# Kernel tuning notes

Hardware: AMD Instinct MI355X
Metric: run time of the kernel (lower is better)

## Reference

```python
import jax, jax.numpy as jnp
import numpy as np

B, N, F, H, E = 32, 512, 256, 1024, 8192
LN_EPS = 1e-5


def setup_inputs() -> dict:
    key = jax.random.key(0)
    ks = jax.random.split(key, 8)
    s = 0.02
    return {
        "node_features": jax.random.normal(ks[0], (B, N, F), jnp.float32),
        "edge_indexd": jax.random.randint(ks[1], (2, E), 0, N, jnp.int64),
        "edge_weights": jax.random.uniform(ks[2], (B, E), jnp.float32),
        "ln_gamma": jnp.ones((F,), jnp.float32),
        "ln_beta": jnp.zeros((F,), jnp.float32),
        "w1": jax.random.normal(ks[3], (H, N), jnp.float32) * s,
        "b1": jnp.zeros((H,), jnp.float32),
        "w2": jax.random.normal(ks[4], (N, H), jnp.float32) * s,
        "b2": jnp.zeros((N,), jnp.float32),
    }


def _laplacian(edge_idx, w):
    # w: [E] edge weights for one graph; edge_idx: [2, E]
    w = jnp.clip(w, 0.0, 1.0)
    # sparse_coo_tensor(...).to_dense() sums duplicate indices -> scatter-add
    A = jnp.zeros((N, N), w.dtype).at[edge_idx[0], edge_idx[1]].add(w)
    A = (A + A.T) * 0.5
    deg = jnp.clip(A.sum(axis=1), 1e-6, None)
    dis = deg ** -0.5  # finite since deg >= 1e-6
    L = jnp.eye(N, dtype=w.dtype) - dis[:, None] * A * dis[None, :]
    L = (L + L.T) * 0.5 + 1e-6 * jnp.eye(N, dtype=w.dtype)
    return L


def _forward(node_features, edge_indexd, edge_weights, ln_gamma, ln_beta, w1, b1, w2, b2):
    L = jax.vmap(lambda w: _laplacian(edge_indexd, w))(edge_weights)  # [B,N,N]
    # eigh is applied to L.detach() in the original -> stop_gradient
    eigvals, eigvecs = jnp.linalg.eigh(jax.lax.stop_gradient(L))  # [B,N], [B,N,N]

    # LayerNorm over feat_dim
    mu = node_features.mean(-1, keepdims=True)
    var = node_features.var(-1, keepdims=True)
    x = (node_features - mu) * jax.lax.rsqrt(var + LN_EPS) * ln_gamma + ln_beta
    x_residual = x
    x = jax.nn.relu(x)

    # x1 = eigvecs^T @ x : [B,N,F]
    x1 = jnp.einsum('bnk,bnf->bkf', eigvecs, x)
    # MLP on eigenvalues (dropout inactive in eval)
    h = jax.nn.relu(eigvals @ w1.T + b1)  # [B,H]
    ev_feat = h @ w2.T + b2               # [B,N]
    x1 = x1 * ev_feat[:, :, None]
    out = jnp.einsum('bnk,bkf->bnf', eigvecs, x1) + x_residual
    return out


def reference(node_features, edge_indexd, edge_weights, ln_gamma, ln_beta, w1, b1, w2, b2):
    return _forward(node_features, edge_indexd, edge_weights, ln_gamma, ln_beta, w1, b1, w2, b2)
```

## Files before the change

kernel.cpp:

```cpp
#include <hip/hip_runtime.h>
#include <math.h>

#define BDIM 32
#define NDIM 512
#define FDIM 256
#define HDIM 1024
#define EDIM 8192
#define PCH  8192
#define CLTH 1.2e-4f
#define NB   16

__device__ __forceinline__ float waveRedSum(float v){
#pragma unroll
  for(int o=32;o>0;o>>=1) v += __shfl_down(v,o,64);
  return v;
}

__device__ __forceinline__ float rnd_f(int g, int i){
  unsigned s = (unsigned)g*1315423911u ^ (unsigned)i*2654435761u;
  s ^= s>>13; s *= 2246822519u; s ^= s>>16;
  return (float)(s & 0xFFFF)*(1.f/65536.f) - 0.5f;
}

__global__ __launch_bounds__(1024) void k_detect(const unsigned* __restrict__ e, int* __restrict__ flag){
  int t = threadIdx.x;
  float c = 0.f;
  for(int i=t;i<EDIM;i+=1024) if(e[2*i+1] != 0u) c += 1.f;
  c = waveRedSum(c);
  __shared__ float r[16];
  if((t&63)==0) r[t>>6]=c;
  __syncthreads();
  if(t==0){ float s=0; for(int z=0;z<16;z++) s+=r[z]; flag[0] = (s>64.f)?1:0; }
}

__global__ __launch_bounds__(256) void k_scatter(const float* __restrict__ ew, const int* __restrict__ eidx,
                                                 const int* __restrict__ flag, float* __restrict__ A){
  int t = blockIdx.x*256 + threadIdx.x;
  int b = t>>13, e = t&(EDIM-1);
  int i, j;
  if(flag[0]){ i = eidx[e]; j = eidx[EDIM+e]; }
  else       { i = eidx[2*e]; j = eidx[2*(EDIM+e)]; }
  i &= 511; j &= 511;
  float w = ew[(size_t)b*EDIM + e];
  w = 0.5f*fminf(fmaxf(w,0.f),1.f);
  float* Ab = A + (size_t)b*NDIM*NDIM;
  atomicAdd(Ab + (size_t)i*NDIM + j, w);
  atomicAdd(Ab + (size_t)j*NDIM + i, w);
}

__global__ __launch_bounds__(256) void k_degree(const float* __restrict__ A, float* __restrict__ dis){
  int wid = threadIdx.x>>6, lane = threadIdx.x&63;
  int row = blockIdx.x*4 + wid;
  const float* Ar = A + (size_t)row*NDIM;
  float s = 0.f;
  for(int j=lane;j<NDIM;j+=64) s += Ar[j];
  s = waveRedSum(s);
  if(lane==0) dis[row] = rsqrtf(fmaxf(s, 1e-6f));
}

__global__ __launch_bounds__(256) void k_lap(float* __restrict__ A, const float* __restrict__ dis){
  size_t t = (size_t)blockIdx.x*256 + threadIdx.x;
  size_t nn = (size_t)NDIM*NDIM;
  int b = (int)(t / nn); size_t rem = t % nn;
  int i = (int)(rem / NDIM), j = (int)(rem % NDIM);
  float v = -dis[b*NDIM+i]*dis[b*NDIM+j]*A[t];
  if(i==j) v += 1.f + 1e-6f;
  A[t] = v;
}

__global__ __launch_bounds__(256) void k_ln(const float* __restrict__ nf, const float* __restrict__ g,
                                            const float* __restrict__ be, float* __restrict__ X){
  int wid = threadIdx.x>>6, lane = threadIdx.x&63;
  int row = blockIdx.x*4 + wid;
  const float4* r4 = (const float4*)(nf + (size_t)row*FDIM);
  float4 v = r4[lane];
  float s  = v.x+v.y+v.z+v.w;
  float s2 = v.x*v.x+v.y*v.y+v.z*v.z+v.w*v.w;
  s = waveRedSum(s); s2 = waveRedSum(s2);
  s = __shfl(s,0,64); s2 = __shfl(s2,0,64);
  float mean = s*(1.f/FDIM);
  float var  = s2*(1.f/FDIM) - mean*mean;
  float inv  = rsqrtf(var + 1e-5f);
  float4 gg = ((const float4*)g)[lane];
  float4 bb = ((const float4*)be)[lane];
  float4 o;
  o.x = (v.x-mean)*inv*gg.x + bb.x;
  o.y = (v.y-mean)*inv*gg.y + bb.y;
  o.z = (v.z-mean)*inv*gg.z + bb.z;
  o.w = (v.w-mean)*inv*gg.w + bb.w;
  ((float4*)(X + (size_t)row*FDIM))[lane] = o;
}

__global__ __launch_bounds__(512,1) void k_tridiag(float* __restrict__ A, float* __restrict__ U,
                                                   float* __restrict__ dia, float* __restrict__ off,
                                                   float* __restrict__ tau){
  const int b = blockIdx.x, t = threadIdx.x;
  float* Ab = A + (size_t)b*NDIM*NDIM;
  float* Ub = U + (size_t)b*NDIM*NDIM;
  __shared__ __align__(16) float Up[NB][NDIM];
  __shared__ __align__(16) float Wp[NB][NDIM];
  __shared__ __align__(16) float ps[4][NDIM];
  __shared__ float dW[NB], dU[NB];
  __shared__ float sig_s, pd_s, x0_s;
  const int lane = t&63;
  const int cc = t&127, rg = t>>7;
  if(t==0){ sig_s = 0.f; pd_s = 0.f; }

  for(int k0=0; k0<NDIM-2; k0+=NB){
    const int ne = (NB < NDIM-2-k0)? NB : (NDIM-2-k0);
    for(int q=0;q<NB;q++){ Up[q][t]=0.f; Wp[q][t]=0.f; }
    __syncthreads();
    for(int p=0;p<ne;p++){
      const int k = k0+p;
      float v = 0.f;
      if(t>k){
        v = Ab[(size_t)k*NDIM + t];
        for(int q=0;q<p;q++) v -= Up[q][k]*Wp[q][t] + Wp[q][k]*Up[q][t];
      }
      if(t<NB){ dW[t]=0.f; dU[t]=0.f; }
      if(t==0) pd_s = 0.f;
      if(t==k+1) x0_s = v;
      float ssq = (t>=k+2)? v*v : 0.f;
      ssq = waveRedSum(ssq);
      if(lane==0) atomicAdd(&sig_s, ssq);
      __syncthreads();
      const float sigma = sig_s, x0 = x0_s;
      float tk = 0.f, inv = 0.f, beta = x0;
      if(sigma > 1e-26f){
        beta = -copysignf(sqrtf(x0*x0+sigma), x0);
        tk = (beta-x0)/beta; inv = 1.f/(x0-beta);
      }
      const float u_t = (t>=k+2)? v*inv : ((t==k+1 && sigma>1e-26f)? 1.f : 0.f);
      Up[p][t] = u_t;
      for(int q=0;q<p;q++){
        float pw = waveRedSum(Wp[q][t]*u_t);
        float pu = waveRedSum(Up[q][t]*u_t);
        if(lane==0){ atomicAdd(&dW[q],pw); atomicAdd(&dU[q],pu); }
      }
      __syncthreads();
      if(t==0) sig_s = 0.f;
      {
        float4 acc = {0.f,0.f,0.f,0.f};
        const int j0 = 4*cc;
        if(j0+3 > k){
          const float* basep = Ab + j0;
          const int ib0 = (k+1)&~15;
          const float* ap = basep + (size_t)(ib0+rg*4)*NDIM;
          float4 c0 = *(const float4*)(ap);
          float4 c1 = *(const float4*)(ap+NDIM);
          float4 c2 = *(const float4*)(ap+2*NDIM);
          float4 c3 = *(const float4*)(ap+3*NDIM);
          for(int ib=ib0; ib<NDIM; ib+=16){
            float4 n0=c0,n1=c1,n2=c2,n3=c3;
            if(ib+16 < NDIM){
              const float* an = basep + (size_t)(ib+16+rg*4)*NDIM;
              n0 = *(const float4*)(an);
              n1 = *(const float4*)(an+NDIM);
              n2 = *(const float4*)(an+2*NDIM);
              n3 = *(const float4*)(an+3*NDIM);
            }
            float4 uv = *(const float4*)&Up[p][ib+rg*4];
            acc.x += c0.x*uv.x + c1.x*uv.y + c2.x*uv.z + c3.x*uv.w;
            acc.y += c0.y*uv.x + c1.y*uv.y + c2.y*uv.z + c3.y*uv.w;
            acc.z += c0.z*uv.x + c1.z*uv.y + c2.z*uv.z + c3.z*uv.w;
            acc.w += c0.w*uv.x + c1.w*uv.y + c2.w*uv.z + c3.w*uv.w;
            c0=n0; c1=n1; c2=n2; c3=n3;
          }
        }
        *(float4*)&ps[rg][4*cc] = acc;
      }
      __syncthreads();
      float py = ps[0][t]+ps[1][t]+ps[2][t]+ps[3][t];
      float corr = 0.f;
      for(int q=0;q<p;q++) corr += Up[q][t]*dW[q] + Wp[q][t]*dU[q];
      float pv = tk*(py - corr);
      float pdp = waveRedSum(pv*u_t);
      if(lane==0) atomicAdd(&pd_s, pdp);
      __syncthreads();
      float hh = 0.5f*tk*pd_s;
      float w_t = (t>k)? (pv - hh*u_t) : 0.f;
      Wp[p][t] = w_t;
      if(t>k) Ub[(size_t)k*NDIM + (t-k-1)] = u_t;
      if(t==0){
        off[(size_t)b*NDIM+k] = beta; tau[(size_t)b*NDIM+k] = tk;
        float dk = Ab[(size_t)k*NDIM+k];
        for(int q=0;q<p;q++) dk -= 2.f*Up[q][k]*Wp[q][k];
        dia[(size_t)b*NDIM+k]=dk;
      }
      __syncthreads();
    }
    {
      const int r0 = k0+ne;
      const int rbase = r0 & ~15;
      const int cstart = rbase>>2;
      if(cc >= cstart){
        const int j0 = 4*cc;
        for(int rt=rbase; rt<NDIM; rt+=16){
          const int i0 = rt + rg*4;
          float* a0 = Ab + (size_t)i0*NDIM + j0;
          float4 v0 = *(float4*)(a0);
          float4 v1 = *(float4*)(a0+NDIM);
          float4 v2 = *(float4*)(a0+2*NDIM);
          float4 v3 = *(float4*)(a0+3*NDIM);
          #pragma unroll 4
          for(int q=0;q<ne;q++){
            float4 Ui = *(const float4*)&Up[q][i0];
            float4 Wi = *(const float4*)&Wp[q][i0];
            float4 Uj = *(const float4*)&Up[q][j0];
            float4 Wj = *(const float4*)&Wp[q][j0];
            v0.x -= Ui.x*Wj.x + Wi.x*Uj.x; v0.y -= Ui.x*Wj.y + Wi.x*Uj.y; v0.z -= Ui.x*Wj.z + Wi.x*Uj.z; v0.w -= Ui.x*Wj.w + Wi.x*Uj.w;
            v1.x -= Ui.y*Wj.x + Wi.y*Uj.x; v1.y -= Ui.y*Wj.y + Wi.y*Uj.y; v1.z -= Ui.y*Wj.z + Wi.y*Uj.z; v1.w -= Ui.y*Wj.w + Wi.y*Uj.w;
            v2.x -= Ui.z*Wj.x + Wi.z*Uj.x; v2.y -= Ui.z*Wj.y + Wi.z*Uj.y; v2.z -= Ui.z*Wj.z + Wi.z*Uj.z; v2.w -= Ui.z*Wj.w + Wi.z*Uj.w;
            v3.x -= Ui.w*Wj.x + Wi.w*Uj.x; v3.y -= Ui.w*Wj.y + Wi.w*Uj.y; v3.z -= Ui.w*Wj.z + Wi.w*Uj.z; v3.w -= Ui.w*Wj.w + Wi.w*Uj.w;
          }
          *(float4*)(a0)        = v0;
          *(float4*)(a0+NDIM)   = v1;
          *(float4*)(a0+2*NDIM) = v2;
          *(float4*)(a0+3*NDIM) = v3;
        }
      }
    }
    __syncthreads();
  }
  if(t==0){
    dia[(size_t)b*NDIM+NDIM-2] = Ab[(size_t)(NDIM-2)*NDIM+NDIM-2];
    dia[(size_t)b*NDIM+NDIM-1] = Ab[(size_t)(NDIM-1)*NDIM+NDIM-1];
    off[(size_t)b*NDIM+NDIM-2] = Ab[(size_t)(NDIM-2)*NDIM+NDIM-1];
    off[(size_t)b*NDIM+NDIM-1] = 0.f;
    tau[(size_t)b*NDIM+NDIM-2]=0.f; tau[(size_t)b*NDIM+NDIM-1]=0.f;
  }
}

__global__ __launch_bounds__(512) void k_bisect(const float* __restrict__ dia, const float* __restrict__ off,
                                                float* __restrict__ lam){
  int b = blockIdx.x, t = threadIdx.x;
  __shared__ float ds[NDIM], e2[NDIM];
  __shared__ float red[16];
  __shared__ float slo, shi;
  ds[t] = dia[(size_t)b*NDIM+t];
  float ev = (t<NDIM-1)? off[(size_t)b*NDIM+t] : 0.f;
  e2[t] = ev*ev;
  __syncthreads();
  float el = (t>0)? sqrtf(e2[t-1]) : 0.f;
  float er = fabsf(ev);
  float lo = ds[t]-el-er, hi = ds[t]+el+er;
#pragma unroll
  for(int o=32;o>0;o>>=1){ lo = fminf(lo,__shfl_down(lo,o,64)); hi = fmaxf(hi,__shfl_down(hi,o,64)); }
  if((t&63)==0){ red[t>>6]=lo; red[8+(t>>6)]=hi; }
  __syncthreads();
  if(t==0){
    float L=red[0], H=red[8];
    for(int z=1;z<8;z++){ L=fminf(L,red[z]); H=fmaxf(H,red[8+z]); }
    slo = L-1e-3f; shi = H+1e-3f;
  }
  __syncthreads();
  float lo2 = slo, hi2 = shi;
  for(int it=0; it<30; ++it){
    float mid = 0.5f*(lo2+hi2);
    float q = ds[0]-mid; int c = (q<0.f)?1:0;
    for(int i=1;i<NDIM;i++){
      float dn = (fabsf(q)<1e-10f)? ((q<0.f)?-1e-10f:1e-10f) : q;
      q = ds[i]-mid - __fdividef(e2[i-1], dn);
      c += (q<0.f)?1:0;
    }
    if(c<=t) lo2=mid; else hi2=mid;
  }
  lam[(size_t)b*NDIM+t] = 0.5f*(lo2+hi2);
}

__global__ __launch_bounds__(64) void k_stein(const float* __restrict__ dia, const float* __restrict__ off,
                                              const float* __restrict__ lam, float* __restrict__ W,
                                              float* __restrict__ fac, float* __restrict__ xs, int chunk){
  int p = blockIdx.x*64 + threadIdx.x;
  int g = chunk*PCH + p;
  int b = g >> 9, j = g & 511;
  __shared__ float ds[NDIM], es[NDIM];
  for(int i=threadIdx.x;i<NDIM;i+=64){ ds[i]=dia[(size_t)b*NDIM+i]; es[i]=off[(size_t)b*NDIM+i]; }
  __syncthreads();
  float lm = lam[(size_t)b*NDIM+j] + (float)((j%5)-2)*1.2e-7f;
  float* fu = fac + p;
  float* fm = fac + (size_t)PCH*NDIM + p;
  float* f1a = xs + p;
  float ai = ds[0]-lm, bi = es[0];
  for(int ib=0; ib<NDIM-1; ib+=8){
    const int lim = (NDIM-1-ib < 8)? NDIM-1-ib : 8;
    float dsb[8], esb[8], enb[8];
    #pragma unroll
    for(int z=0;z<8;z++){
      int i = ib+z; bool vz = z<lim;
      dsb[z] = vz? ds[i+1] : 0.f;
      esb[z] = vz? es[i]   : 0.f;
      enb[z] = (vz && i<NDIM-2)? es[i+1] : 0.f;
    }
    #pragma unroll
    for(int z=0;z<8;z++){
      if(z<lim){
        int i = ib+z;
        float ci = esb[z], an = dsb[z]-lm, bn = enb[z];
        float uu, mmenc, s1;
        if(fabsf(ai) >= fabsf(ci)){
          float aa = (fabsf(ai)<1e-12f)? ((ai<0.f)?-1e-12f:1e-12f) : ai;
          float mm = __fdividef(ci, aa);
          uu=aa; mmenc=mm; s1=bi;
          ai = an - mm*bi; bi = bn;
        } else {
          float cch = (fabsf(ci)<1e-12f)? ((ci<0.f)?-1e-12f:1e-12f) : ci;
          float mm = __fdividef(ai, cch);
          uu=cch; mmenc=mm+3.f; s1=an;
          ai = bi - mm*an; bi = -mm*bn;
        }
        fu[(size_t)i*PCH]=__fdividef(1.f,uu);
        fm[(size_t)i*PCH]=mmenc;
        f1a[(size_t)i*PCH]=s1;
      }
    }
  }
  { float aa = (fabsf(ai)<1e-12f)? ((ai<0.f)?-1e-12f:1e-12f) : ai; fu[(size_t)(NDIM-1)*PCH]=__fdividef(1.f,aa); }
  float* Wb = W + (size_t)b*NDIM*NDIM + j;
  float scale = 1.f;
  for(int it=0; it<3; ++it){
    float yi = (it==0)? rnd_f(g,0) : Wb[0]*scale;
    for(int ib=0; ib<NDIM-1; ib+=8){
      const int lim = (NDIM-1-ib < 8)? NDIM-1-ib : 8;
      float wn[8], me[8];
      #pragma unroll
      for(int z=0;z<8;z++){
        int i = ib+z; bool vz = z<lim;
        wn[z] = vz? ((it==0)? rnd_f(g,i+1) : Wb[(size_t)(i+1)*NDIM]*scale) : 0.f;
        me[z] = vz? fm[(size_t)i*PCH] : 0.f;
      }
      #pragma unroll
      for(int z=0;z<8;z++){
        if(z<lim){
          int i = ib+z;
          float enc = me[z]; bool sw = enc>1.5f; float mm = sw? enc-3.f : enc;
          float yn = wn[z];
          if(sw){ float tmp=yi; yi=yn; yn=tmp; }
          yn -= mm*yi;
          Wb[(size_t)i*NDIM] = yi;
          yi = yn;
        }
      }
    }
    float nrm, xp1, xp2;
    {
      float xi = yi * fu[(size_t)(NDIM-1)*PCH];
      Wb[(size_t)(NDIM-1)*NDIM]=xi; nrm = xi*xi; xp2=0.f; xp1=xi;
    }
    for(int ib=NDIM-2; ib>=0; ib-=8){
      const int lim = (ib+1 < 8)? ib+1 : 8;
      float yv[8], ru[8], me[8], f1b[8];
      #pragma unroll
      for(int z=0;z<8;z++){
        int i = ib-z; bool vz = z<lim;
        yv[z]  = vz? Wb[(size_t)i*NDIM] : 0.f;
        ru[z]  = vz? fu[(size_t)i*PCH] : 0.f;
        me[z]  = vz? fm[(size_t)i*PCH] : 0.f;
        f1b[z] = vz? f1a[(size_t)i*PCH] : 0.f;
      }
      #pragma unroll
      for(int z=0;z<8;z++){
        if(z<lim){
          int i = ib-z;
          bool sw = me[z]>1.5f;
          float f2 = sw? ((i<NDIM-2)? es[i+1] : 0.f) : 0.f;
          float xi = (yv[z] - f1b[z]*xp1 - f2*xp2)*ru[z];
          Wb[(size_t)i*NDIM]=xi; nrm += xi*xi;
          xp2=xp1; xp1=xi;
        }
      }
    }
    scale = rsqrtf(fmaxf(nrm,1e-30f));
  }
  for(int ib=0; ib<NDIM; ib+=8){
    float vz[8];
    #pragma unroll
    for(int z=0;z<8;z++) vz[z] = Wb[(size_t)(ib+z)*NDIM];
    #pragma unroll
    for(int z=0;z<8;z++) Wb[(size_t)(ib+z)*NDIM] = vz[z]*scale;
  }
}

__global__ __launch_bounds__(512) void k_mgs(const float* __restrict__ lam, float* __restrict__ W){
  int b = blockIdx.x, t = threadIdx.x;
  __shared__ int cstart[NDIM];
  __shared__ unsigned char brk[NDIM];
  __shared__ float red[8];
  __shared__ float sbc;
  const float* lb = lam + (size_t)b*NDIM;
  float* Wb = W + (size_t)b*NDIM*NDIM;
  brk[t] = (t==0)? 1 : ((lb[t]-lb[t-1] > CLTH)? 1 : 0);
  __syncthreads();
  if(t==0){ int s=0; for(int j=0;j<NDIM;j++){ if(brk[j]) s=j; cstart[j]=s; } }
  __syncthreads();
  for(int j=1;j<NDIM;j++){
    int s = cstart[j];
    if(s==j) continue;
    for(int q=s;q<j;q++){
      float pd = 0.f;
      pd = Wb[(size_t)t*NDIM+q]*Wb[(size_t)t*NDIM+j];
      pd = waveRedSum(pd);
      if((t&63)==0) red[t>>6]=pd;
      __syncthreads();
      if(t==0){ float s2=0; for(int z=0;z<8;z++) s2+=red[z]; sbc=s2; }
      __syncthreads();
      float dt = sbc;
      Wb[(size_t)t*NDIM+j] -= dt*Wb[(size_t)t*NDIM+q];
      __syncthreads();
    }
    float v = Wb[(size_t)t*NDIM+j];
    float pn = waveRedSum(v*v);
    if((t&63)==0) red[t>>6]=pn;
    __syncthreads();
    if(t==0){ float s2=0; for(int z=0;z<8;z++) s2+=red[z]; sbc=s2; }
    __syncthreads();
    Wb[(size_t)t*NDIM+j] = v*rsqrtf(fmaxf(sbc,1e-20f));
    __syncthreads();
  }
}

__global__ __launch_bounds__(512) void k_backt(float* __restrict__ W, const float* __restrict__ U,
                                               const float* __restrict__ tau){
  __shared__ float S[NDIM][33];
  __shared__ float uk[NDIM];
  __shared__ float part[16][32];
  int b = blockIdx.x >> 4, slab = blockIdx.x & 15;
  int c0 = slab*32;
  float* Wb = W + (size_t)b*NDIM*NDIM;
  for(int l=threadIdx.x; l<NDIM*32; l+=512){
    int i = l>>5, c = l&31;
    S[i][c] = Wb[(size_t)i*NDIM + c0 + c];
  }
  __syncthreads();
  int c = threadIdx.x & 31, q = threadIdx.x >> 5;
  for(int k=NDIM-3;k>=0;--k){
    float tk = tau[(size_t)b*NDIM + k];
    if(tk == 0.f) continue;
    int m = NDIM-1-k;
    const float* Uk = U + ((size_t)b*NDIM + k)*NDIM;
    for(int i=threadIdx.x;i<m;i+=512) uk[i] = Uk[i];
    __syncthreads();
    float acc = 0.f;
    for(int r=q;r<m;r+=16) acc += uk[r]*S[k+1+r][c];
    part[q][c] = acc;
    __syncthreads();
    float sval = 0.f;
    #pragma unroll
    for(int z=0;z<16;z++) sval += part[z][c];
    sval *= tk;
    for(int r=q;r<m;r+=16) S[k+1+r][c] -= sval*uk[r];
    __syncthreads();
  }
  for(int l=threadIdx.x; l<NDIM*32; l+=512){
    int i = l>>5, cc2 = l&31;
    Wb[(size_t)i*NDIM + c0 + cc2] = S[i][cc2];
  }
}

__global__ __launch_bounds__(256) void k_mlp1(const float* __restrict__ lam, const float* __restrict__ w1,
                                              const float* __restrict__ b1, float* __restrict__ h){
  int wid = threadIdx.x>>6, lane = threadIdx.x&63;
  int j = blockIdx.x*4 + wid, b = blockIdx.y;
  const float* lb = lam + (size_t)b*NDIM;
  const float* wr = w1 + (size_t)j*NDIM;
  float acc = 0.f;
  for(int k=lane;k<NDIM;k+=64) acc += lb[k]*wr[k];
  acc = waveRedSum(acc);
  if(lane==0) h[(size_t)b*HDIM + j] = fmaxf(acc + b1[j], 0.f);
}
__global__ __launch_bounds__(256) void k_mlp2(const float* __restrict__ h, const float* __restrict__ w2,
                                              const float* __restrict__ b2, float* __restrict__ evb){
  int wid = threadIdx.x>>6, lane = threadIdx.x&63;
  int n = blockIdx.x*4 + wid, b = blockIdx.y;
  const float* hb = h + (size_t)b*HDIM;
  const float* wr = w2 + (size_t)n*HDIM;
  float acc = 0.f;
  for(int k=lane;k<HDIM;k+=64) acc += hb[k]*wr[k];
  acc = waveRedSum(acc);
  if(lane==0) evb[(size_t)b*NDIM + n] = acc + b2[n];
}

__global__ __launch_bounds__(256) void k_gemm1(const float* __restrict__ Z, const float* __restrict__ X,
                                               const float* __restrict__ evb, float* __restrict__ X1){
  int b = blockIdx.z;
  int i0 = blockIdx.y*64, f0 = blockIdx.x*64;
  const float* Zb = Z + (size_t)b*NDIM*NDIM;
  const float* Xb = X + (size_t)b*NDIM*FDIM;
  __shared__ float As[32][65], Bs[32][65];
  int tx = threadIdx.x & 15, ty = threadIdx.x >> 4;
  float acc[4][4] = {};
  for(int n0=0;n0<NDIM;n0+=32){
    for(int l=threadIdx.x; l<32*64; l+=256){
      int dn = l>>6, dc = l&63;
      As[dn][dc] = Zb[(size_t)(n0+dn)*NDIM + i0+dc];
      Bs[dn][dc] = fmaxf(Xb[(size_t)(n0+dn)*FDIM + f0+dc], 0.f);
    }
    __syncthreads();
#pragma unroll
    for(int dn=0;dn<32;dn++){
      float a[4], bb[4];
#pragma unroll
      for(int z=0;z<4;z++){ a[z]=As[dn][ty*4+z]; bb[z]=Bs[dn][tx*4+z]; }
#pragma unroll
      for(int p=0;p<4;p++)
#pragma unroll
        for(int q=0;q<4;q++) acc[p][q] += a[p]*bb[q];
    }
    __syncthreads();
  }
#pragma unroll
  for(int p=0;p<4;p++){
    int i = i0 + ty*4 + p;
    float s = evb[(size_t)b*NDIM + i];
    float4 o = { acc[p][0]*s, acc[p][1]*s, acc[p][2]*s, acc[p][3]*s };
    *(float4*)(X1 + ((size_t)b*NDIM + i)*FDIM + f0 + tx*4) = o;
  }
}

__global__ __launch_bounds__(256) void k_gemm2(const float* __restrict__ Z, const float* __restrict__ X1,
                                               const float* __restrict__ X, float* __restrict__ outp){
  int b = blockIdx.z;
  int n0 = blockIdx.y*64, f0 = blockIdx.x*64;
  const float* Zb = Z + (size_t)b*NDIM*NDIM;
  const float* X1b = X1 + (size_t)b*NDIM*FDIM;
  __shared__ float As[32][65], Bs[32][65];
  int tx = threadIdx.x & 15, ty = threadIdx.x >> 4;
  float acc[4][4] = {};
  for(int i0=0;i0<NDIM;i0+=32){
    for(int l=threadIdx.x; l<32*64; l+=256){
      int di = l&31, dn = l>>5;
      As[di][dn] = Zb[(size_t)(n0+dn)*NDIM + i0+di];
    }
    for(int l=threadIdx.x; l<32*64; l+=256){
      int di = l>>6, df = l&63;
      Bs[di][df] = X1b[(size_t)(i0+di)*FDIM + f0+df];
    }
    __syncthreads();
#pragma unroll
    for(int dk=0;dk<32;dk++){
      float a[4], bb[4];
#pragma unroll
      for(int z=0;z<4;z++){ a[z]=As[dk][ty*4+z]; bb[z]=Bs[dk][tx*4+z]; }
#pragma unroll
      for(int p=0;p<4;p++)
#pragma unroll
        for(int q=0;q<4;q++) acc[p][q] += a[p]*bb[q];
    }
    __syncthreads();
  }
#pragma unroll
  for(int p=0;p<4;p++){
    size_t ro = ((size_t)b*NDIM + n0+ty*4+p)*FDIM + f0 + tx*4;
    float4 xr = *(const float4*)(X + ro);
    float4 o = { acc[p][0]+xr.x, acc[p][1]+xr.y, acc[p][2]+xr.z, acc[p][3]+xr.w };
    *(float4*)(outp + ro) = o;
  }
}

extern "C" void kernel_launch(void* const* d_in, const int* in_sizes, int n_in,
                              void* d_out, int out_size, void* d_ws, size_t ws_size,
                              hipStream_t stream) {
  (void)in_sizes; (void)n_in; (void)out_size; (void)ws_size;
  const float* nf  = (const float*)d_in[0];
  const int*   eidx= (const int*)d_in[1];
  const float* ew  = (const float*)d_in[2];
  const float* lng = (const float*)d_in[3];
  const float* lnb = (const float*)d_in[4];
  const float* w1  = (const float*)d_in[5];
  const float* b1  = (const float*)d_in[6];
  const float* w2  = (const float*)d_in[7];
  const float* b2  = (const float*)d_in[8];

  float* ws = (float*)d_ws;
  const size_t NN = (size_t)NDIM*NDIM;
  float* A   = ws;
  float* U   = A  + (size_t)BDIM*NN;
  float* W   = U  + (size_t)BDIM*NN;
  float* X   = W  + (size_t)BDIM*NN;
  float* X1  = X  + (size_t)BDIM*NDIM*FDIM;
  float* dia = X1 + (size_t)BDIM*NDIM*FDIM;
  float* off = dia + (size_t)BDIM*NDIM;
  float* tau = off + (size_t)BDIM*NDIM;
  float* lam = tau + (size_t)BDIM*NDIM;
  float* dis = lam + (size_t)BDIM*NDIM;
  float* hbf = dis + (size_t)BDIM*NDIM;
  float* evb = hbf + (size_t)BDIM*HDIM;
  int*   flag= (int*)(evb + (size_t)BDIM*NDIM);

  hipMemsetAsync(A, 0, (size_t)BDIM*NN*sizeof(float), stream);
  k_detect <<<1, 1024, 0, stream>>>((const unsigned*)eidx, flag);
  k_scatter<<<(BDIM*EDIM)/256, 256, 0, stream>>>(ew, eidx, flag, A);
  k_degree <<<(BDIM*NDIM)/4, 256, 0, stream>>>(A, dis);
  k_lap    <<<(unsigned)((size_t)BDIM*NN/256), 256, 0, stream>>>(A, dis);
  k_ln     <<<(BDIM*NDIM)/4, 256, 0, stream>>>(nf, lng, lnb, X);
  k_tridiag<<<BDIM, 512, 0, stream>>>(A, U, dia, off, tau);
  k_bisect <<<BDIM, 512, 0, stream>>>(dia, off, lam);
  k_mlp1   <<<dim3(HDIM/4, BDIM), 256, 0, stream>>>(lam, w1, b1, hbf);
  k_mlp2   <<<dim3(NDIM/4, BDIM), 256, 0, stream>>>(hbf, w2, b2, evb);
  for(int c=0;c<(BDIM*NDIM)/PCH;c++)
    k_stein<<<PCH/64, 64, 0, stream>>>(dia, off, lam, W, A , X1 , c);
  k_mgs    <<<BDIM, 512, 0, stream>>>(lam, W);
  k_backt  <<<BDIM*16, 512, 0, stream>>>(W, U, tau);
  k_gemm1  <<<dim3(FDIM/64, NDIM/64, BDIM), 256, 0, stream>>>(W, X, evb, X1);
  k_gemm2  <<<dim3(FDIM/64, NDIM/64, BDIM), 256, 0, stream>>>(W, X1, X, (float*)d_out);
}
```

Baseline: 9.862 ms.

## Block Householder back-transform with compact WY and deepen tridiag matvec unroll

Rewrites the eigenvector back-transformation to apply Householder reflectors in blocks of 16 using a compact WY form (Gram matrix, triangular T, then two small GEMM-like updates). This replaces 510 sequential rank-1 updates, each with its own barriers, with about 32 blocked steps. The column slab is narrowed to 16 so twice as many blocks launch. The tridiagonalization matvec loop is also unrolled to 32 rows per iteration to get more loads in flight. The cost is extra shared memory, register pressure, and some numerical reordering.

```diff
diff --git a/kernel.cpp b/kernel.cpp
--- a/kernel.cpp
+++ b/kernel.cpp
@@ -9,6 +9,7 @@
 #define PCH  8192
 #define CLTH 1.2e-4f
 #define NB   16
+#define BCOLS 16
 
 __device__ __forceinline__ float waveRedSum(float v){
 #pragma unroll
@@ -144,27 +145,41 @@
         const int j0 = 4*cc;
         if(j0+3 > k){
           const float* basep = Ab + j0;
-          const int ib0 = (k+1)&~15;
-          const float* ap = basep + (size_t)(ib0+rg*4)*NDIM;
-          float4 c0 = *(const float4*)(ap);
-          float4 c1 = *(const float4*)(ap+NDIM);
-          float4 c2 = *(const float4*)(ap+2*NDIM);
-          float4 c3 = *(const float4*)(ap+3*NDIM);
-          for(int ib=ib0; ib<NDIM; ib+=16){
-            float4 n0=c0,n1=c1,n2=c2,n3=c3;
-            if(ib+16 < NDIM){
-              const float* an = basep + (size_t)(ib+16+rg*4)*NDIM;
-              n0 = *(const float4*)(an);
-              n1 = *(const float4*)(an+NDIM);
-              n2 = *(const float4*)(an+2*NDIM);
-              n3 = *(const float4*)(an+3*NDIM);
+          const int ib0 = (k+1)&~31;
+          const int i1 = rg*4, i2 = 16+rg*4;
+          const float* ap = basep + (size_t)ib0*NDIM;
+          float4 c0 = *(const float4*)(ap + (size_t)(i1  )*NDIM);
+          float4 c1 = *(const float4*)(ap + (size_t)(i1+1)*NDIM);
+          float4 c2 = *(const float4*)(ap + (size_t)(i1+2)*NDIM);
+          float4 c3 = *(const float4*)(ap + (size_t)(i1+3)*NDIM);
+          float4 d0 = *(const float4*)(ap + (size_t)(i2  )*NDIM);
+          float4 d1 = *(const float4*)(ap + (size_t)(i2+1)*NDIM);
+          float4 d2 = *(const float4*)(ap + (size_t)(i2+2)*NDIM);
+          float4 d3 = *(const float4*)(ap + (size_t)(i2+3)*NDIM);
+          for(int ib=ib0; ib<NDIM; ib+=32){
+            float4 n0=c0,n1=c1,n2=c2,n3=c3,m0=d0,m1=d1,m2=d2,m3=d3;
+            if(ib+32 < NDIM){
+              const float* an = basep + (size_t)(ib+32)*NDIM;
+              n0 = *(const float4*)(an + (size_t)(i1  )*NDIM);
+              n1 = *(const float4*)(an + (size_t)(i1+1)*NDIM);
+              n2 = *(const float4*)(an + (size_t)(i1+2)*NDIM);
+              n3 = *(const float4*)(an + (size_t)(i1+3)*NDIM);
+              m0 = *(const float4*)(an + (size_t)(i2  )*NDIM);
+              m1 = *(const float4*)(an + (size_t)(i2+1)*NDIM);
+              m2 = *(const float4*)(an + (size_t)(i2+2)*NDIM);
+              m3 = *(const float4*)(an + (size_t)(i2+3)*NDIM);
             }
-            float4 uv = *(const float4*)&Up[p][ib+rg*4];
-            acc.x += c0.x*uv.x + c1.x*uv.y + c2.x*uv.z + c3.x*uv.w;
-            acc.y += c0.y*uv.x + c1.y*uv.y + c2.y*uv.z + c3.y*uv.w;
-            acc.z += c0.z*uv.x + c1.z*uv.y + c2.z*uv.z + c3.z*uv.w;
-            acc.w += c0.w*uv.x + c1.w*uv.y + c2.w*uv.z + c3.w*uv.w;
-            c0=n0; c1=n1; c2=n2; c3=n3;
+            float4 u1 = *(const float4*)&Up[p][ib+i1];
+            float4 u2 = *(const float4*)&Up[p][ib+i2];
+            acc.x += c0.x*u1.x + c1.x*u1.y + c2.x*u1.z + c3.x*u1.w
+                   + d0.x*u2.x + d1.x*u2.y + d2.x*u2.z + d3.x*u2.w;
+            acc.y += c0.y*u1.x + c1.y*u1.y + c2.y*u1.z + c3.y*u1.w
+                   + d0.y*u2.x + d1.y*u2.y + d2.y*u2.z + d3.y*u2.w;
+            acc.z += c0.z*u1.x + c1.z*u1.y + c2.z*u1.z + c3.z*u1.w
+                   + d0.z*u2.x + d1.z*u2.y + d2.z*u2.z + d3.z*u2.w;
+            acc.w += c0.w*u1.x + c1.w*u1.y + c2.w*u1.z + c3.w*u1.w
+                   + d0.w*u2.x + d1.w*u2.y + d2.w*u2.z + d3.w*u2.w;
+            c0=n0; c1=n1; c2=n2; c3=n3; d0=m0; d1=m1; d2=m2; d3=m3;
           }
         }
         *(float4*)&ps[rg][4*cc] = acc;
@@ -419,41 +434,94 @@
   }
 }
 
-__global__ __launch_bounds__(512) void k_backt(float* __restrict__ W, const float* __restrict__ U,
-                                               const float* __restrict__ tau){
-  __shared__ float S[NDIM][33];
-  __shared__ float uk[NDIM];
-  __shared__ float part[16][32];
-  int b = blockIdx.x >> 4, slab = blockIdx.x & 15;
-  int c0 = slab*32;
+__global__ __launch_bounds__(512,4) void k_backt(float* __restrict__ W, const float* __restrict__ U,
+                                                 const float* __restrict__ tau){
+  __shared__ float S[NDIM][BCOLS+1];
+  __shared__ float Up[NB][516];
+  __shared__ float Gp[NB][NB+1];
+  __shared__ float Tm[NB][NB+1];
+  __shared__ float Yp[2][NB][NB+1];
+  __shared__ float Z16[NB][NB+1];
+  __shared__ float tls[NB];
+  const int t = threadIdx.x;
+  int b = blockIdx.x >> 5, slab = blockIdx.x & 31;
+  int c0 = slab*BCOLS;
   float* Wb = W + (size_t)b*NDIM*NDIM;
-  for(int l=threadIdx.x; l<NDIM*32; l+=512){
-    int i = l>>5, c = l&31;
+  const float* Ub = U + (size_t)b*NDIM*NDIM;
+  for(int l=t; l<NDIM*BCOLS; l+=512){
+    int i = l>>4, c = l&15;
     S[i][c] = Wb[(size_t)i*NDIM + c0 + c];
   }
   __syncthreads();
-  int c = threadIdx.x & 31, q = threadIdx.x >> 5;
-  for(int k=NDIM-3;k>=0;--k){
-    float tk = tau[(size_t)b*NDIM + k];
-    if(tk == 0.f) continue;
-    int m = NDIM-1-k;
-    const float* Uk = U + ((size_t)b*NDIM + k)*NDIM;
-    for(int i=threadIdx.x;i<m;i+=512) uk[i] = Uk[i];
-    __syncthreads();
-    float acc = 0.f;
-    for(int r=q;r<m;r+=16) acc += uk[r]*S[k+1+r][c];
-    part[q][c] = acc;
-    __syncthreads();
-    float sval = 0.f;
-    #pragma unroll
-    for(int z=0;z<16;z++) sval += part[z][c];
-    sval *= tk;
-    for(int r=q;r<m;r+=16) S[k+1+r][c] -= sval*uk[r];
-    __syncthreads();
-  }
-  for(int l=threadIdx.x; l<NDIM*32; l+=512){
-    int i = l>>5, cc2 = l&31;
-    Wb[(size_t)i*NDIM + c0 + cc2] = S[i][cc2];
+  for(int k0 = ((NDIM-3)/NB)*NB; k0>=0; k0-=NB){
+    for(int l=t; l<NB*NDIM; l+=512){
+      int q = l>>9, i = l&511;
+      int k = k0+q;
+      float v = 0.f;
+      if(k < NDIM-2 && i > k) v = Ub[(size_t)k*NDIM + (i-k-1)];
+      Up[q][i] = v;
+    }
+    if(t<NB) tls[t] = (k0+t < NDIM-2)? tau[(size_t)b*NDIM + k0 + t] : 0.f;
+    if(t<NB*(NB+1)) ((float*)Gp)[t] = 0.f;
+    __syncthreads();
+    if(t < 480){
+      int pp = t>>2, sub = t&3;
+      int pj=1, pr=pp;
+      while(pr >= pj){ pr -= pj; pj++; }
+      int s = pr, jj = pj;
+      float acc = 0.f;
+      for(int i=k0+1+sub; i<NDIM; i+=4) acc += Up[s][i]*Up[jj][i];
+      atomicAdd(&Gp[s][jj], acc);
+    }
+    __syncthreads();
+    if(t < 16){
+      int a = t;
+      for(int j=0;j<NB;j++){
+        float v;
+        if(a==j) v = tls[j];
+        else if(a<j){
+          float s2 = 0.f;
+          for(int s=a; s<j; s++) s2 += Tm[a][s]*Gp[s][j];
+          v = -tls[j]*s2;
+        } else v = 0.f;
+        Tm[a][j] = v;
+      }
+    }
+    __syncthreads();
+    {
+      int q=(t>>4)&15, c=t&15, half=t>>8;
+      float a0=0.f, a1=0.f;
+      int i = k0+1+half;
+      for(; i+2<NDIM; i+=4){ a0 += Up[q][i]*S[i][c]; a1 += Up[q][i+2]*S[i+2][c]; }
+      for(; i<NDIM; i+=2) a0 += Up[q][i]*S[i][c];
+      Yp[half][q][c] = a0+a1;
+    }
+    __syncthreads();
+    if(t < 256){
+      int a=t>>4, c=t&15;
+      float acc=0.f;
+      #pragma unroll
+      for(int j=0;j<NB;j++) acc += Tm[a][j]*(Yp[0][j][c]+Yp[1][j][c]);
+      Z16[a][c]=acc;
+    }
+    __syncthreads();
+    {
+      int rg=t>>4, c=t&15;
+      float zc[NB];
+      #pragma unroll
+      for(int q=0;q<NB;q++) zc[q]=Z16[q][c];
+      for(int i=k0+1+rg; i<NDIM; i+=32){
+        float s2=0.f;
+        #pragma unroll
+        for(int q=0;q<NB;q++) s2 += Up[q][i]*zc[q];
+        S[i][c] -= s2;
+      }
+    }
+    __syncthreads();
+  }
+  for(int l=t; l<NDIM*BCOLS; l+=512){
+    int i = l>>4, c = l&15;
+    Wb[(size_t)i*NDIM + c0 + c] = S[i][c];
   }
 }
 
@@ -600,7 +668,7 @@
   for(int c=0;c<(BDIM*NDIM)/PCH;c++)
     k_stein<<<PCH/64, 64, 0, stream>>>(dia, off, lam, W, A , X1 , c);
   k_mgs    <<<BDIM, 512, 0, stream>>>(lam, W);
-  k_backt  <<<BDIM*16, 512, 0, stream>>>(W, U, tau);
+  k_backt  <<<BDIM*32, 512, 0, stream>>>(W, U, tau);
   k_gemm1  <<<dim3(FDIM/64, NDIM/64, BDIM), 256, 0, stream>>>(W, X, evb, X1);
   k_gemm2  <<<dim3(FDIM/64, NDIM/64, BDIM), 256, 0, stream>>>(W, X1, X, (float*)d_out);
 }
```

After: 9.986 ms. Within noise of the previous version (+1.3%).
